# Performance work log

Hardware: AMD Instinct MI355X
Metric: run time of the kernel (lower is better)

Reference implementation:

```python
import jax, jax.numpy as jnp
import numpy as np

N_NODES = 100000
N_EDGES = 3200000
IN_FEATS = 256
N_UNITS = 32
OUT_FEATS = 40


def setup_inputs() -> dict:
    key = jax.random.key(0)
    k = jax.random.split(key, 6)
    return {
        "x": jax.random.normal(k[0], (N_NODES, IN_FEATS), dtype=jnp.float32),
        "W1": jax.random.normal(k[1], (IN_FEATS, N_UNITS), dtype=jnp.float32) / np.sqrt(IN_FEATS),
        "b1": jnp.zeros((N_UNITS,), dtype=jnp.float32),
        "W2": jax.random.normal(k[2], (N_UNITS, OUT_FEATS), dtype=jnp.float32) / np.sqrt(N_UNITS),
        "b2": jnp.zeros((OUT_FEATS,), dtype=jnp.float32),
        "src": jax.random.randint(k[3], (N_EDGES,), 0, N_NODES, dtype=jnp.int32),
        "dst": jax.random.randint(k[4], (N_EDGES,), 0, N_NODES, dtype=jnp.int32),
    }


def _graph_conv(x, W, b, src, dst, inv_sqrt_out, inv_sqrt_in, n_nodes):
    # DGL GraphConv, norm='both':
    #   out = D_in^{-1/2} * A^T * (D_out^{-1/2} * x @ W) + b
    # Apply the dense transform first (in_feats >= out_feats here) so edge
    # messages are gathered at the narrow width.
    h = (x * inv_sqrt_out[:, None]) @ W              # [N, F_out]
    msgs = h[src]                                     # [E, F_out] gather
    agg = jax.ops.segment_sum(msgs, dst, num_segments=n_nodes)  # [N, F_out]
    return agg * inv_sqrt_in[:, None] + b


def reference(x, W1, b1, W2, b2, src, dst):
    n = x.shape[0]
    ones = jnp.ones((src.shape[0],), dtype=x.dtype)
    out_deg = jax.ops.segment_sum(ones, src, num_segments=n)
    in_deg = jax.ops.segment_sum(ones, dst, num_segments=n)
    inv_sqrt_out = jax.lax.rsqrt(jnp.maximum(out_deg, 1.0))  # DGL clamps deg>=1
    inv_sqrt_in = jax.lax.rsqrt(jnp.maximum(in_deg, 1.0))

    h = _graph_conv(x, W1, b1, src, dst, inv_sqrt_out, inv_sqrt_in, n)
    h = jax.nn.relu(h)
    # dropout(p=0.5, training=False) is identity in eval mode
    h = _graph_conv(h, W2, b2, src, dst, inv_sqrt_out, inv_sqrt_in, n)
    return jax.nn.log_softmax(h, axis=1)
```

## Files before the change

### kernel.cpp

```cpp
#include <hip/hip_runtime.h>
#include <hip/hip_bf16.h>
#include <math.h>

#define N_NODES 100000
#define N_EDGES 3200000
#define IN_FEATS 256
#define N_UNITS 32
#define OUT_FEATS 40

#define NPB 64
#define BSHIFT 6
#define NB 1563
#define CAP 4096

#define NC 49
#define CSHIFT 11
#define CHUNK 8192
#define NBLK ((N_EDGES + CHUNK - 1) / CHUNK)
#define WIN 128

#define ODS2 65536
#define OD_WORDS 16384
#define OD_NSL 2
#define OD_S 192
#define HIST_NBLK (OD_NSL * OD_S)
#define COUNT_NBLK 128

#define GHALF 391
#define NSPLIT (GHALF * 128)

__global__ void __launch_bounds__(256) histcount_kernel(const int* __restrict__ src,
                                                        const int* __restrict__ dst,
                                                        unsigned* __restrict__ partials,
                                                        int* __restrict__ bucket_count) {
    __shared__ __align__(16) char smem[OD_WORDS * 4];
    int tid = threadIdx.x;
    if (blockIdx.x < HIST_NBLK) {
        unsigned* lh = (unsigned*)smem;
        int slice = blockIdx.x / OD_S;
        int stripe = blockIdx.x % OD_S;
        for (int i = tid; i < OD_WORDS; i += 256) lh[i] = 0;
        __syncthreads();
        int lo = slice * ODS2;
        const int4* s4 = (const int4*)src;
        const int total4 = N_EDGES / 4;
        for (int i = stripe * 256 + tid; i < total4; i += OD_S * 256) {
            int4 v = s4[i];
            unsigned a = (unsigned)(v.x - lo); if (a < ODS2) atomicAdd(&lh[a >> 2], 1u << ((a & 3) * 8));
            unsigned b = (unsigned)(v.y - lo); if (b < ODS2) atomicAdd(&lh[b >> 2], 1u << ((b & 3) * 8));
            unsigned c = (unsigned)(v.z - lo); if (c < ODS2) atomicAdd(&lh[c >> 2], 1u << ((c & 3) * 8));
            unsigned d = (unsigned)(v.w - lo); if (d < ODS2) atomicAdd(&lh[d >> 2], 1u << ((d & 3) * 8));
        }
        __syncthreads();
        unsigned* dstp = partials + (size_t)blockIdx.x * OD_WORDS;
        for (int i = tid; i < OD_WORDS; i += 256) dstp[i] = lh[i];
    } else {
        int* lh = (int*)smem;
        int cb = blockIdx.x - HIST_NBLK;
        for (int i = tid; i < NB; i += 256) lh[i] = 0;
        __syncthreads();
        const int4* d4 = (const int4*)dst;
        const int total4 = N_EDGES / 4;
        for (int i = cb * 256 + tid; i < total4; i += COUNT_NBLK * 256) {
            int4 v = d4[i];
            atomicAdd(&lh[v.x >> BSHIFT], 1);
            atomicAdd(&lh[v.y >> BSHIFT], 1);
            atomicAdd(&lh[v.z >> BSHIFT], 1);
            atomicAdd(&lh[v.w >> BSHIFT], 1);
        }
        __syncthreads();
        for (int i = tid; i < NB; i += 256)
            if (lh[i]) atomicAdd(&bucket_count[i], lh[i]);
    }
}

__global__ void __launch_bounds__(1024) scanreduce_kernel(const int* __restrict__ bucket_count,
                                                          int* __restrict__ gbase,
                                                          int* __restrict__ gcursor,
                                                          int* __restrict__ gbaseA,
                                                          int* __restrict__ gcursorA,
                                                          const unsigned* __restrict__ partials,
                                                          float* __restrict__ inv_out) {
    __shared__ int ps[1024];
    int t = threadIdx.x;
    if (blockIdx.x == 0) {
        int i0 = 2 * t, i1 = 2 * t + 1;
        int a = (i0 < NB) ? bucket_count[i0] : 0;
        int b = (i1 < NB) ? bucket_count[i1] : 0;
        ps[t] = a + b;
        __syncthreads();
        for (int off = 1; off < 1024; off <<= 1) {
            int v = (t >= off) ? ps[t - off] : 0;
            __syncthreads();
            ps[t] += v;
            __syncthreads();
        }
        int excl = ps[t] - (a + b);
        if (i0 < NB) { gbase[i0] = excl; gcursor[i0] = excl; }
        if (i1 <= NB) { gbase[i1] = excl + a; if (i1 < NB) gcursor[i1] = excl + a; }
        __syncthreads();
        if (t < NC) { int v = gbase[t * 32]; gbaseA[t] = v; gcursorA[t] = v; }
        if (t == NC) gbaseA[NC] = N_EDGES;
    } else {
        int i = (blockIdx.x - 1) * 1024 + t;
        if (i >= N_NODES / 4) return;
        int slice = i >> 14;
        int w = i & (OD_WORDS - 1);
        const unsigned* p = partials + (size_t)slice * OD_S * OD_WORDS + w;
        unsigned s = 0;
        #pragma unroll 8
        for (int j = 0; j < OD_S; ++j) s += p[(size_t)j * OD_WORDS];
        float4 r;
        r.x = rsqrtf(fmaxf((float)(s & 0xFF), 1.0f));
        r.y = rsqrtf(fmaxf((float)((s >> 8) & 0xFF), 1.0f));
        r.z = rsqrtf(fmaxf((float)((s >> 16) & 0xFF), 1.0f));
        r.w = rsqrtf(fmaxf((float)(s >> 24), 1.0f));
        *(float4*)(inv_out + 4 * i) = r;
    }
}

__device__ __forceinline__ void gemm_body(char* smem, int tid, int gblk,
                                          const float* __restrict__ x,
                                          const float* __restrict__ W1,
                                          const float* __restrict__ inv_out,
                                          float* __restrict__ h, int nbase) {
    float* Ws = (float*)smem;
    for (int idx = tid; idx < IN_FEATS * N_UNITS / 4; idx += 512)
        ((float4*)Ws)[idx] = ((const float4*)W1)[idx];
    __syncthreads();
    unsigned n = (unsigned)(nbase + gblk * 128) + (tid >> 2);
    if (n >= (unsigned)N_NODES) return;
    unsigned j0 = (tid & 3) * 8;
    float acc[8] = {0, 0, 0, 0, 0, 0, 0, 0};
    const float4* xr = (const float4*)(x + (size_t)n * IN_FEATS);
    #pragma unroll 4
    for (int k4 = 0; k4 < IN_FEATS / 4; ++k4) {
        float4 xv = xr[k4];
        const float* wk = Ws + (k4 * 4) * N_UNITS + j0;
        #pragma unroll
        for (int jj = 0; jj < 8; ++jj) acc[jj] = fmaf(xv.x, wk[jj], acc[jj]);
        #pragma unroll
        for (int jj = 0; jj < 8; ++jj) acc[jj] = fmaf(xv.y, wk[N_UNITS + jj], acc[jj]);
        #pragma unroll
        for (int jj = 0; jj < 8; ++jj) acc[jj] = fmaf(xv.z, wk[2 * N_UNITS + jj], acc[jj]);
        #pragma unroll
        for (int jj = 0; jj < 8; ++jj) acc[jj] = fmaf(xv.w, wk[3 * N_UNITS + jj], acc[jj]);
    }
    float io = inv_out[n];
    float* hr = h + (size_t)n * N_UNITS + j0;
    #pragma unroll
    for (int jj = 0; jj < 8; ++jj) hr[jj] = acc[jj] * io;
}

__global__ void __launch_bounds__(512) binAgemm_kernel(const int* __restrict__ src,
                                                       const int* __restrict__ dst,
                                                       int* __restrict__ gcursorA,
                                                       unsigned* __restrict__ pairsA,
                                                       const float* __restrict__ x,
                                                       const float* __restrict__ W1,
                                                       const float* __restrict__ inv_out,
                                                       float* __restrict__ h) {
    __shared__ __align__(16) char smem[CHUNK * 4 + 4 * NC * 4];
    int tid = threadIdx.x;
    if (blockIdx.x < GHALF) {
        gemm_body(smem, tid, blockIdx.x, x, W1, inv_out, h, 0);
        return;
    }
    unsigned* sortedA = (unsigned*)smem;
    int* hist   = (int*)(smem + CHUNK * 4);
    int* lstart = hist + NC;
    int* cur    = lstart + NC;
    int* gres   = cur + NC;
    int e0 = (blockIdx.x - GHALF) * CHUNK;
    int cnt = min(CHUNK, N_EDGES - e0);
    unsigned es[16], ed[16];
    #pragma unroll
    for (int r = 0; r < 16; ++r) {
        int idx = tid + 512 * r;
        if (idx < cnt) { es[r] = src[e0 + idx]; ed[r] = dst[e0 + idx]; }
    }
    if (tid < NC) hist[tid] = 0;
    __syncthreads();
    #pragma unroll
    for (int r = 0; r < 16; ++r) {
        int idx = tid + 512 * r;
        if (idx < cnt) atomicAdd(&hist[ed[r] >> CSHIFT], 1);
    }
    __syncthreads();
    if (tid < 64) {
        int v = (tid < NC) ? hist[tid] : 0;
        int inc = v;
        #pragma unroll
        for (int off = 1; off < 64; off <<= 1) {
            int u = __shfl_up(inc, off, 64);
            if ((tid & 63) >= off) inc += u;
        }
        if (tid < NC) {
            int ls = inc - v;
            lstart[tid] = ls;
            cur[tid] = ls;
            gres[tid] = atomicAdd(&gcursorA[tid], v) - ls;
        }
    }
    __syncthreads();
    #pragma unroll
    for (int r = 0; r < 16; ++r) {
        int idx = tid + 512 * r;
        if (idx < cnt) {
            int c = ed[r] >> CSHIFT;
            int pos = atomicAdd(&cur[c], 1);
            sortedA[pos] = es[r] | ((ed[r] & ((1u << CSHIFT) - 1)) << 17);
        }
    }
    __syncthreads();
    for (int i = tid; i < cnt; i += 512) {
        int lo = 0, hi = NC - 1;
        while (lo < hi) { int mid = (lo + hi + 1) >> 1; if (lstart[mid] <= i) lo = mid; else hi = mid - 1; }
        pairsA[gres[lo] + i] = sortedA[i];
    }
}

__global__ void __launch_bounds__(512) binBgemm_kernel(const unsigned* __restrict__ pairsA,
                                                       const int* __restrict__ gbaseA,
                                                       int* __restrict__ gcursor,
                                                       unsigned* __restrict__ pairs,
                                                       const float* __restrict__ x,
                                                       const float* __restrict__ W1,
                                                       const float* __restrict__ inv_out,
                                                       float* __restrict__ h) {
    __shared__ __align__(16) char smem[CHUNK * 4 + 4 * WIN * 4 + (NC + 2) * 4];
    int tid = threadIdx.x;
    if (blockIdx.x < GHALF) {
        gemm_body(smem, tid, blockIdx.x, x, W1, inv_out, h, NSPLIT);
        return;
    }
    unsigned* sortedB = (unsigned*)smem;
    int* hist   = (int*)(smem + CHUNK * 4);
    int* lstart = hist + WIN;
    int* cur    = lstart + WIN;
    int* gres   = cur + WIN;
    int* gA     = gres + WIN;
    if (tid <= NC) gA[tid] = gbaseA[tid];
    if (tid < WIN) hist[tid] = 0;
    int e0 = (blockIdx.x - GHALF) * CHUNK;
    int cnt = min(CHUNK, N_EDGES - e0);
    __syncthreads();
    int c0 = 0;
    { int lo = 0, hi = NC - 1;
      while (lo < hi) { int mid = (lo + hi + 1) >> 1; if (gA[mid] <= e0) lo = mid; else hi = mid - 1; }
      c0 = lo; }
    int w0 = c0 * 32;
    unsigned pv[16]; short fw[16];
    int c = c0;
    #pragma unroll
    for (int r = 0; r < 16; ++r) {
        int idx = tid + 512 * r;
        if (idx < cnt) {
            int pos = e0 + idx;
            while (pos >= gA[c + 1]) ++c;
            unsigned p = pairsA[pos];
            unsigned srcid = p & 0x1FFFF;
            unsigned dl11 = (p >> 17) & 0x7FF;
            int wi = (c - c0) * 32 + (int)(dl11 >> 6);
            atomicAdd(&hist[wi], 1);
            pv[r] = srcid | ((dl11 & 63u) << 24);
            fw[r] = (short)wi;
        }
    }
    __syncthreads();
    if (tid < 64) {
        int v0 = hist[2 * tid], v1 = hist[2 * tid + 1];
        int s = v0 + v1;
        int inc = s;
        #pragma unroll
        for (int off = 1; off < 64; off <<= 1) {
            int u = __shfl_up(inc, off, 64);
            if ((tid & 63) >= off) inc += u;
        }
        int excl = inc - s;
        lstart[2 * tid] = excl;      cur[2 * tid] = excl;
        lstart[2 * tid + 1] = excl + v0; cur[2 * tid + 1] = excl + v0;
        int f0 = w0 + 2 * tid, f1 = f0 + 1;
        gres[2 * tid]     = (f0 < NB) ? (atomicAdd(&gcursor[f0], v0) - excl) : 0;
        gres[2 * tid + 1] = (f1 < NB) ? (atomicAdd(&gcursor[f1], v1) - (excl + v0)) : 0;
    }
    __syncthreads();
    #pragma unroll
    for (int r = 0; r < 16; ++r) {
        int idx = tid + 512 * r;
        if (idx < cnt) {
            int pos = atomicAdd(&cur[fw[r]], 1);
            sortedB[pos] = pv[r];
        }
    }
    __syncthreads();
    for (int i = tid; i < cnt; i += 512) {
        int lo = 0, hi = WIN - 1;
        while (lo < hi) { int mid = (lo + hi + 1) >> 1; if (lstart[mid] <= i) lo = mid; else hi = mid - 1; }
        pairs[gres[lo] + i] = sortedB[i];
    }
}

template <bool LAYER1>
__global__ void __launch_bounds__(256) gather_kernel(
        const float* __restrict__ in, const unsigned* __restrict__ pairs,
        const int* __restrict__ gbase, const float* __restrict__ inv_out,
        const float* __restrict__ b1, float* __restrict__ outbuf,
        float* __restrict__ inv_in) {
    __shared__ int sorted[CAP];
    __shared__ int cnt[NPB];
    __shared__ int start[NPB + 1];
    __shared__ int cur[NPB];
    __shared__ float b1s[N_UNITS];
    int tid = threadIdx.x;
    int b = blockIdx.x;
    int ebeg = gbase[b];
    int ecnt = min(gbase[b + 1] - ebeg, CAP);
    if (tid < NPB) cnt[tid] = 0;
    if (LAYER1 && tid < N_UNITS) b1s[tid] = b1[tid];
    __syncthreads();

    unsigned stash[16];
    #pragma unroll
    for (int r = 0; r < 16; ++r) {
        int idx = tid + 256 * r;
        if (idx < ecnt) {
            unsigned p = pairs[ebeg + idx];
            stash[r] = p;
            atomicAdd(&cnt[p >> 24], 1);
        }
    }
    __syncthreads();

    if (tid < 64) {
        int v = cnt[tid];
        int inc = v;
        #pragma unroll
        for (int off = 1; off < 64; off <<= 1) {
            int u = __shfl_up(inc, off, 64);
            if (tid >= off) inc += u;
        }
        start[tid + 1] = inc;
        cur[tid] = inc - v;
        if (tid == 0) start[0] = 0;
    }
    __syncthreads();

    #pragma unroll
    for (int r = 0; r < 16; ++r) {
        int idx = tid + 256 * r;
        if (idx < ecnt) {
            unsigned p = stash[r];
            int pos = atomicAdd(&cur[p >> 24], 1);
            sorted[pos] = (int)(p & 0xFFFFFF);
        }
    }
    __syncthreads();

    int w = tid >> 6;
    int lane = tid & 63;
    int q = lane & 7;
    int eo = lane >> 3;
    int nd0 = b * NPB;
    #pragma unroll 1
    for (int p = 0; p < 16; ++p) {
        int nd = w * 16 + p;
        int n = nd0 + nd;
        int beg = start[nd];
        int end = start[nd + 1];
        float ax0 = 0.f, ay0 = 0.f, az0 = 0.f, aw0 = 0.f;
        float ax1 = 0.f, ay1 = 0.f, az1 = 0.f, aw1 = 0.f;
        int e = beg + eo;
        for (; e + 8 < end; e += 16) {
            int s0 = sorted[e];
            int s1 = sorted[e + 8];
            float4 v0 = *(const float4*)(in + (size_t)s0 * N_UNITS + q * 4);
            float4 v1 = *(const float4*)(in + (size_t)s1 * N_UNITS + q * 4);
            ax0 += v0.x; ay0 += v0.y; az0 += v0.z; aw0 += v0.w;
            ax1 += v1.x; ay1 += v1.y; az1 += v1.z; aw1 += v1.w;
        }
        if (e < end) {
            float4 v = *(const float4*)(in + (size_t)sorted[e] * N_UNITS + q * 4);
            ax0 += v.x; ay0 += v.y; az0 += v.z; aw0 += v.w;
        }
        e += 8;
        if (e < end) {
            float4 v = *(const float4*)(in + (size_t)sorted[e] * N_UNITS + q * 4);
            ax1 += v.x; ay1 += v.y; az1 += v.z; aw1 += v.w;
        }
        float sx = ax0 + ax1, sy = ay0 + ay1, sz = az0 + az1, sw = aw0 + aw1;
        #pragma unroll
        for (int st = 8; st < 64; st <<= 1) {
            sx += __shfl_xor(sx, st, 64);
            sy += __shfl_xor(sy, st, 64);
            sz += __shfl_xor(sz, st, 64);
            sw += __shfl_xor(sw, st, 64);
        }
        if (eo == 0 && n < N_NODES) {
            if (LAYER1) {
                float ii = rsqrtf(fmaxf((float)(end - beg), 1.0f));
                float io = inv_out[n];
                float4 r;
                r.x = fmaxf(fmaf(sx, ii, b1s[q * 4 + 0]), 0.0f) * io;
                r.y = fmaxf(fmaf(sy, ii, b1s[q * 4 + 1]), 0.0f) * io;
                r.z = fmaxf(fmaf(sz, ii, b1s[q * 4 + 2]), 0.0f) * io;
                r.w = fmaxf(fmaf(sw, ii, b1s[q * 4 + 3]), 0.0f) * io;
                *(float4*)(outbuf + (size_t)n * N_UNITS + q * 4) = r;
                if (q == 0) inv_in[n] = ii;
            } else {
                *(float4*)(outbuf + (size_t)n * N_UNITS + q * 4) =
                    make_float4(sx, sy, sz, sw);
            }
        }
    }
}

__global__ void __launch_bounds__(256) finalize_kernel(
        const float* __restrict__ agg2, const float* __restrict__ inv_in,
        const float* __restrict__ W2, const float* __restrict__ b2,
        float* __restrict__ out, int N) {
    __shared__ float W2s[N_UNITS * OUT_FEATS];
    __shared__ float b2s[OUT_FEATS];
    for (int i = threadIdx.x; i < N_UNITS * OUT_FEATS; i += 256) W2s[i] = W2[i];
    if (threadIdx.x < OUT_FEATS) b2s[threadIdx.x] = b2[threadIdx.x];
    __syncthreads();
    int n = blockIdx.x * 256 + threadIdx.x;
    if (n >= N) return;
    float a[N_UNITS];
    const float4* ar = (const float4*)(agg2 + (size_t)n * N_UNITS);
    #pragma unroll
    for (int qq = 0; qq < N_UNITS / 4; ++qq) {
        float4 v = ar[qq];
        a[qq * 4 + 0] = v.x; a[qq * 4 + 1] = v.y; a[qq * 4 + 2] = v.z; a[qq * 4 + 3] = v.w;
    }
    float ii = inv_in[n];
    float s[OUT_FEATS];
    #pragma unroll
    for (int o = 0; o < OUT_FEATS; ++o) s[o] = 0.0f;
    #pragma unroll
    for (int k = 0; k < N_UNITS; ++k) {
        float ak = a[k];
        #pragma unroll
        for (int o = 0; o < OUT_FEATS; ++o) s[o] = fmaf(ak, W2s[k * OUT_FEATS + o], s[o]);
    }
    float mx = -INFINITY;
    #pragma unroll
    for (int o = 0; o < OUT_FEATS; ++o) {
        s[o] = fmaf(s[o], ii, b2s[o]);
        mx = fmaxf(mx, s[o]);
    }
    float sum = 0.0f;
    #pragma unroll
    for (int o = 0; o < OUT_FEATS; ++o) sum += __expf(s[o] - mx);
    float lse = mx + __logf(sum);
    #pragma unroll
    for (int o = 0; o < OUT_FEATS; ++o) s[o] -= lse;
    float4* orow4 = (float4*)(out + (size_t)n * OUT_FEATS);
    #pragma unroll
    for (int qq = 0; qq < OUT_FEATS / 4; ++qq)
        orow4[qq] = make_float4(s[qq * 4], s[qq * 4 + 1], s[qq * 4 + 2], s[qq * 4 + 3]);
}

extern "C" void kernel_launch(void* const* d_in, const int* in_sizes, int n_in,
                              void* d_out, int out_size, void* d_ws, size_t ws_size,
                              hipStream_t stream) {
    const float* x   = (const float*)d_in[0];
    const float* W1  = (const float*)d_in[1];
    const float* b1  = (const float*)d_in[2];
    const float* W2  = (const float*)d_in[3];
    const float* b2  = (const float*)d_in[4];
    const int*   src = (const int*)d_in[5];
    const int*   dst = (const int*)d_in[6];
    float* out = (float*)d_out;

    char* base = (char*)d_ws;
    float*    inv_out      = (float*)(base);
    int*      bucket_count = (int*)(base + 400000L);
    int*      gbaseA       = (int*)(base + 406400L);
    int*      gcursorA     = (int*)(base + 406912L);
    int*      gbase        = (int*)(base + 408192L);
    int*      gcursor      = (int*)(base + 416384L);
    float*    inv_in       = (float*)(base + 424576L);
    unsigned* pairs        = (unsigned*)(base + 824576L);
    unsigned* pairsA       = (unsigned*)(base + 13624576L);
    float*    rprime       = (float*)(base + 26424576L);
    float*    h            = (float*)(base + 39224576L);
    float*    agg2         = (float*)(base + 39224576L);
    unsigned* partials     = (unsigned*)rprime;

    hipMemsetAsync(bucket_count, 0, 8192L, stream);

    histcount_kernel<<<HIST_NBLK + COUNT_NBLK, 256, 0, stream>>>(src, dst, partials, bucket_count);
    scanreduce_kernel<<<1 + (N_NODES / 4 + 1023) / 1024, 1024, 0, stream>>>(
        bucket_count, gbase, gcursor, gbaseA, gcursorA, partials, inv_out);

    binAgemm_kernel<<<GHALF + NBLK, 512, 0, stream>>>(
        src, dst, gcursorA, pairsA, x, W1, inv_out, h);
    binBgemm_kernel<<<GHALF + NBLK, 512, 0, stream>>>(
        pairsA, gbaseA, gcursor, pairs, x, W1, inv_out, h);

    gather_kernel<true><<<NB, 256, 0, stream>>>(h, pairs, gbase, inv_out, b1, rprime, inv_in);
    gather_kernel<false><<<NB, 256, 0, stream>>>(rprime, pairs, gbase, inv_out, b1, agg2, inv_in);

    finalize_kernel<<<(N_NODES + 255) / 256, 256, 0, stream>>>(agg2, inv_in, W2, b2, out, N_NODES);
}
```

Before: 359.8 us.

## Replace sliced shared-memory out-degree histogram with direct global atomics

Out-degrees are now counted with global integer atomics on a zeroed array, in the same pass that builds the dst bucket histogram. This replaces the two-slice packed-byte shared-memory histogram, its partials buffer and the reduction in the scan kernel. The inverse square root is computed on the fly wherever the out-degree is consumed. This drops one full read of src, the partials write and reduce, and simplifies the scan kernel. The cost is 3.2M global atomics spread over 100K addresses, which can contend, plus a larger memset.

```diff
diff --git a/kernel.cpp b/kernel.cpp
--- a/kernel.cpp
+++ b/kernel.cpp
@@ -19,110 +19,68 @@
 #define NBLK ((N_EDGES + CHUNK - 1) / CHUNK)
 #define WIN 128
 
-#define ODS2 65536
-#define OD_WORDS 16384
-#define OD_NSL 2
-#define OD_S 192
-#define HIST_NBLK (OD_NSL * OD_S)
-#define COUNT_NBLK 128
-
 #define GHALF 391
 #define NSPLIT (GHALF * 128)
 
-__global__ void __launch_bounds__(256) histcount_kernel(const int* __restrict__ src,
+#define EC_NBLK 512
+
+__global__ void __launch_bounds__(256) edgecount_kernel(const int* __restrict__ src,
                                                         const int* __restrict__ dst,
-                                                        unsigned* __restrict__ partials,
+                                                        int* __restrict__ outdeg,
                                                         int* __restrict__ bucket_count) {
-    __shared__ __align__(16) char smem[OD_WORDS * 4];
-    int tid = threadIdx.x;
-    if (blockIdx.x < HIST_NBLK) {
-        unsigned* lh = (unsigned*)smem;
-        int slice = blockIdx.x / OD_S;
-        int stripe = blockIdx.x % OD_S;
-        for (int i = tid; i < OD_WORDS; i += 256) lh[i] = 0;
-        __syncthreads();
-        int lo = slice * ODS2;
-        const int4* s4 = (const int4*)src;
-        const int total4 = N_EDGES / 4;
-        for (int i = stripe * 256 + tid; i < total4; i += OD_S * 256) {
-            int4 v = s4[i];
-            unsigned a = (unsigned)(v.x - lo); if (a < ODS2) atomicAdd(&lh[a >> 2], 1u << ((a & 3) * 8));
-            unsigned b = (unsigned)(v.y - lo); if (b < ODS2) atomicAdd(&lh[b >> 2], 1u << ((b & 3) * 8));
-            unsigned c = (unsigned)(v.z - lo); if (c < ODS2) atomicAdd(&lh[c >> 2], 1u << ((c & 3) * 8));
-            unsigned d = (unsigned)(v.w - lo); if (d < ODS2) atomicAdd(&lh[d >> 2], 1u << ((d & 3) * 8));
-        }
-        __syncthreads();
-        unsigned* dstp = partials + (size_t)blockIdx.x * OD_WORDS;
-        for (int i = tid; i < OD_WORDS; i += 256) dstp[i] = lh[i];
-    } else {
-        int* lh = (int*)smem;
-        int cb = blockIdx.x - HIST_NBLK;
-        for (int i = tid; i < NB; i += 256) lh[i] = 0;
-        __syncthreads();
-        const int4* d4 = (const int4*)dst;
-        const int total4 = N_EDGES / 4;
-        for (int i = cb * 256 + tid; i < total4; i += COUNT_NBLK * 256) {
-            int4 v = d4[i];
-            atomicAdd(&lh[v.x >> BSHIFT], 1);
-            atomicAdd(&lh[v.y >> BSHIFT], 1);
-            atomicAdd(&lh[v.z >> BSHIFT], 1);
-            atomicAdd(&lh[v.w >> BSHIFT], 1);
-        }
-        __syncthreads();
-        for (int i = tid; i < NB; i += 256)
-            if (lh[i]) atomicAdd(&bucket_count[i], lh[i]);
-    }
-}
-
-__global__ void __launch_bounds__(1024) scanreduce_kernel(const int* __restrict__ bucket_count,
-                                                          int* __restrict__ gbase,
-                                                          int* __restrict__ gcursor,
-                                                          int* __restrict__ gbaseA,
-                                                          int* __restrict__ gcursorA,
-                                                          const unsigned* __restrict__ partials,
-                                                          float* __restrict__ inv_out) {
+    __shared__ int lh[NB];
+    for (int i = threadIdx.x; i < NB; i += 256) lh[i] = 0;
+    __syncthreads();
+    const int4* s4 = (const int4*)src;
+    const int4* d4 = (const int4*)dst;
+    const int total4 = N_EDGES / 4;
+    for (int i = blockIdx.x * 256 + threadIdx.x; i < total4; i += EC_NBLK * 256) {
+        int4 s = s4[i];
+        int4 v = d4[i];
+        atomicAdd(&outdeg[s.x], 1);
+        atomicAdd(&outdeg[s.y], 1);
+        atomicAdd(&outdeg[s.z], 1);
+        atomicAdd(&outdeg[s.w], 1);
+        atomicAdd(&lh[v.x >> BSHIFT], 1);
+        atomicAdd(&lh[v.y >> BSHIFT], 1);
+        atomicAdd(&lh[v.z >> BSHIFT], 1);
+        atomicAdd(&lh[v.w >> BSHIFT], 1);
+    }
+    __syncthreads();
+    for (int i = threadIdx.x; i < NB; i += 256)
+        if (lh[i]) atomicAdd(&bucket_count[i], lh[i]);
+}
+
+__global__ void __launch_bounds__(1024) scan_kernel(const int* __restrict__ bucket_count,
+                                                    int* __restrict__ gbase,
+                                                    int* __restrict__ gcursor,
+                                                    int* __restrict__ gbaseA,
+                                                    int* __restrict__ gcursorA) {
     __shared__ int ps[1024];
     int t = threadIdx.x;
-    if (blockIdx.x == 0) {
-        int i0 = 2 * t, i1 = 2 * t + 1;
-        int a = (i0 < NB) ? bucket_count[i0] : 0;
-        int b = (i1 < NB) ? bucket_count[i1] : 0;
-        ps[t] = a + b;
+    int i0 = 2 * t, i1 = 2 * t + 1;
+    int a = (i0 < NB) ? bucket_count[i0] : 0;
+    int b = (i1 < NB) ? bucket_count[i1] : 0;
+    ps[t] = a + b;
+    __syncthreads();
+    for (int off = 1; off < 1024; off <<= 1) {
+        int v = (t >= off) ? ps[t - off] : 0;
         __syncthreads();
-        for (int off = 1; off < 1024; off <<= 1) {
-            int v = (t >= off) ? ps[t - off] : 0;
-            __syncthreads();
-            ps[t] += v;
-            __syncthreads();
-        }
-        int excl = ps[t] - (a + b);
-        if (i0 < NB) { gbase[i0] = excl; gcursor[i0] = excl; }
-        if (i1 <= NB) { gbase[i1] = excl + a; if (i1 < NB) gcursor[i1] = excl + a; }
+        ps[t] += v;
         __syncthreads();
-        if (t < NC) { int v = gbase[t * 32]; gbaseA[t] = v; gcursorA[t] = v; }
-        if (t == NC) gbaseA[NC] = N_EDGES;
-    } else {
-        int i = (blockIdx.x - 1) * 1024 + t;
-        if (i >= N_NODES / 4) return;
-        int slice = i >> 14;
-        int w = i & (OD_WORDS - 1);
-        const unsigned* p = partials + (size_t)slice * OD_S * OD_WORDS + w;
-        unsigned s = 0;
-        #pragma unroll 8
-        for (int j = 0; j < OD_S; ++j) s += p[(size_t)j * OD_WORDS];
-        float4 r;
-        r.x = rsqrtf(fmaxf((float)(s & 0xFF), 1.0f));
-        r.y = rsqrtf(fmaxf((float)((s >> 8) & 0xFF), 1.0f));
-        r.z = rsqrtf(fmaxf((float)((s >> 16) & 0xFF), 1.0f));
-        r.w = rsqrtf(fmaxf((float)(s >> 24), 1.0f));
-        *(float4*)(inv_out + 4 * i) = r;
-    }
+    }
+    int excl = ps[t] - (a + b);
+    if (i0 < NB) { gbase[i0] = excl; gcursor[i0] = excl; }
+    if (i1 <= NB) { gbase[i1] = excl + a; if (i1 < NB) gcursor[i1] = excl + a; }
+    __syncthreads();
+    if (t < NC) { int v = gbase[t * 32]; gbaseA[t] = v; gcursorA[t] = v; }
+    if (t == NC) gbaseA[NC] = N_EDGES;
 }
 
 __device__ __forceinline__ void gemm_body(char* smem, int tid, int gblk,
                                           const float* __restrict__ x,
                                           const float* __restrict__ W1,
-                                          const float* __restrict__ inv_out,
+                                          const int* __restrict__ outdeg,
                                           float* __restrict__ h, int nbase) {
     float* Ws = (float*)smem;
     for (int idx = tid; idx < IN_FEATS * N_UNITS / 4; idx += 512)
@@ -146,7 +104,7 @@
         #pragma unroll
         for (int jj = 0; jj < 8; ++jj) acc[jj] = fmaf(xv.w, wk[3 * N_UNITS + jj], acc[jj]);
     }
-    float io = inv_out[n];
+    float io = rsqrtf(fmaxf((float)outdeg[n], 1.0f));
     float* hr = h + (size_t)n * N_UNITS + j0;
     #pragma unroll
     for (int jj = 0; jj < 8; ++jj) hr[jj] = acc[jj] * io;
@@ -158,12 +116,12 @@
                                                        unsigned* __restrict__ pairsA,
                                                        const float* __restrict__ x,
                                                        const float* __restrict__ W1,
-                                                       const float* __restrict__ inv_out,
+                                                       const int* __restrict__ outdeg,
                                                        float* __restrict__ h) {
     __shared__ __align__(16) char smem[CHUNK * 4 + 4 * NC * 4];
     int tid = threadIdx.x;
     if (blockIdx.x < GHALF) {
-        gemm_body(smem, tid, blockIdx.x, x, W1, inv_out, h, 0);
+        gemm_body(smem, tid, blockIdx.x, x, W1, outdeg, h, 0);
         return;
     }
     unsigned* sortedA = (unsigned*)smem;
@@ -226,12 +184,12 @@
                                                        unsigned* __restrict__ pairs,
                                                        const float* __restrict__ x,
                                                        const float* __restrict__ W1,
-                                                       const float* __restrict__ inv_out,
+                                                       const int* __restrict__ outdeg,
                                                        float* __restrict__ h) {
     __shared__ __align__(16) char smem[CHUNK * 4 + 4 * WIN * 4 + (NC + 2) * 4];
     int tid = threadIdx.x;
     if (blockIdx.x < GHALF) {
-        gemm_body(smem, tid, blockIdx.x, x, W1, inv_out, h, NSPLIT);
+        gemm_body(smem, tid, blockIdx.x, x, W1, outdeg, h, NSPLIT);
         return;
     }
     unsigned* sortedB = (unsigned*)smem;
@@ -304,7 +262,7 @@
 template <bool LAYER1>
 __global__ void __launch_bounds__(256) gather_kernel(
         const float* __restrict__ in, const unsigned* __restrict__ pairs,
-        const int* __restrict__ gbase, const float* __restrict__ inv_out,
+        const int* __restrict__ gbase, const int* __restrict__ outdeg,
         const float* __restrict__ b1, float* __restrict__ outbuf,
         float* __restrict__ inv_in) {
     __shared__ int sorted[CAP];
@@ -399,7 +357,7 @@
         if (eo == 0 && n < N_NODES) {
             if (LAYER1) {
                 float ii = rsqrtf(fmaxf((float)(end - beg), 1.0f));
-                float io = inv_out[n];
+                float io = rsqrtf(fmaxf((float)outdeg[n], 1.0f));
                 float4 r;
                 r.x = fmaxf(fmaf(sx, ii, b1s[q * 4 + 0]), 0.0f) * io;
                 r.y = fmaxf(fmaf(sy, ii, b1s[q * 4 + 1]), 0.0f) * io;
@@ -474,7 +432,7 @@
     float* out = (float*)d_out;
 
     char* base = (char*)d_ws;
-    float*    inv_out      = (float*)(base);
+    int*      outdeg       = (int*)(base);
     int*      bucket_count = (int*)(base + 400000L);
     int*      gbaseA       = (int*)(base + 406400L);
     int*      gcursorA     = (int*)(base + 406912L);
@@ -486,21 +444,19 @@
     float*    rprime       = (float*)(base + 26424576L);
     float*    h            = (float*)(base + 39224576L);
     float*    agg2         = (float*)(base + 39224576L);
-    unsigned* partials     = (unsigned*)rprime;
-
-    hipMemsetAsync(bucket_count, 0, 8192L, stream);
-
-    histcount_kernel<<<HIST_NBLK + COUNT_NBLK, 256, 0, stream>>>(src, dst, partials, bucket_count);
-    scanreduce_kernel<<<1 + (N_NODES / 4 + 1023) / 1024, 1024, 0, stream>>>(
-        bucket_count, gbase, gcursor, gbaseA, gcursorA, partials, inv_out);
+
+    hipMemsetAsync(base, 0, 408192L, stream);
+
+    edgecount_kernel<<<EC_NBLK, 256, 0, stream>>>(src, dst, outdeg, bucket_count);
+    scan_kernel<<<1, 1024, 0, stream>>>(bucket_count, gbase, gcursor, gbaseA, gcursorA);
 
     binAgemm_kernel<<<GHALF + NBLK, 512, 0, stream>>>(
-        src, dst, gcursorA, pairsA, x, W1, inv_out, h);
+        src, dst, gcursorA, pairsA, x, W1, outdeg, h);
     binBgemm_kernel<<<GHALF + NBLK, 512, 0, stream>>>(
-        pairsA, gbaseA, gcursor, pairs, x, W1, inv_out, h);
-
-    gather_kernel<true><<<NB, 256, 0, stream>>>(h, pairs, gbase, inv_out, b1, rprime, inv_in);
-    gather_kernel<false><<<NB, 256, 0, stream>>>(rprime, pairs, gbase, inv_out, b1, agg2, inv_in);
+        pairsA, gbaseA, gcursor, pairs, x, W1, outdeg, h);
+
+    gather_kernel<true><<<NB, 256, 0, stream>>>(h, pairs, gbase, outdeg, b1, rprime, inv_in);
+    gather_kernel<false><<<NB, 256, 0, stream>>>(rprime, pairs, gbase, outdeg, b1, agg2, inv_in);
 
     finalize_kernel<<<(N_NODES + 255) / 256, 256, 0, stream>>>(agg2, inv_in, W2, b2, out, N_NODES);
 }
```

Result: slower. 469.1 us (+30.4%).
